# Performance work log

Measured on AMD Instinct MI355X. Metric: run time of the kernel, lower is better.

## Reference

```python
import jax, jax.numpy as jnp
import numpy as np

DROPOUT_P = 0.5
NUM_NODES = 50000


def _gcn_layer(x, W, b, src, dst, ew, num_nodes):
    # support = x @ W ; out = A_hat @ support + b, with A_hat given as edge list
    h = x @ W                               # [N, out_dim]
    msg = h[src] * ew[:, None]              # [E, out_dim]
    agg = jax.ops.segment_sum(msg, dst, num_segments=num_nodes)  # [N, out_dim]
    return agg + b


def setup_inputs() -> dict:
    key = jax.random.key(0)
    ks = jax.random.split(key, 8)
    N, E, F_in, H, C = NUM_NODES, 800000, 512, 128, 64
    x = jax.random.normal(ks[0], (N, F_in), dtype=jnp.float32)
    edge_weight = jax.random.uniform(ks[1], (E,), dtype=jnp.float32)
    W1 = jax.random.normal(ks[2], (F_in, H), dtype=jnp.float32) * (1.0 / np.sqrt(F_in))
    b1 = jax.random.normal(ks[3], (H,), dtype=jnp.float32) * 0.01
    W2 = jax.random.normal(ks[4], (H, C), dtype=jnp.float32) * (1.0 / np.sqrt(H))
    b2 = jax.random.normal(ks[5], (C,), dtype=jnp.float32) * 0.01
    drop_mask = jax.random.uniform(ks[6], (N, H), dtype=jnp.float32)
    edge_index = jax.random.randint(ks[7], (2, E), 0, N, dtype=jnp.int32)
    return {"x": x, "edge_weight": edge_weight, "W1": W1, "b1": b1,
            "W2": W2, "b2": b2, "drop_mask": drop_mask, "edge_index": edge_index}


def reference(x, edge_weight, W1, b1, W2, b2, drop_mask, edge_index):
    src, dst = edge_index[0], edge_index[1]
    h = _gcn_layer(x, W1, b1, src, dst, edge_weight, NUM_NODES)
    h = jax.nn.relu(h)
    # deterministic inverted dropout using precomputed uniform mask
    keep = (drop_mask >= DROPOUT_P).astype(h.dtype)
    h = h * keep / (1.0 - DROPOUT_P)
    h = _gcn_layer(h, W2, b2, src, dst, edge_weight, NUM_NODES)
    return jax.nn.log_softmax(h, axis=1)
```

## Files before the change

kernel.cpp:

```cpp
#include <hip/hip_runtime.h>
#include <cstdint>
#include <cstddef>

constexpr int FIN = 512;
constexpr int HD  = 128;
constexpr int CD  = 64;

typedef __attribute__((ext_vector_type(8))) short short8;
typedef __attribute__((ext_vector_type(4))) float f32x4;

__device__ inline unsigned short f2bf(float f) {
  unsigned int u = __float_as_uint(f);
  u += 0x7fffu + ((u >> 16) & 1u);
  return (unsigned short)(u >> 16);
}
__device__ inline float bf_lo(unsigned int v) { return __uint_as_float(v << 16); }
__device__ inline float bf_hi(unsigned int v) { return __uint_as_float(v & 0xffff0000u); }
__device__ inline float bf1(unsigned short v) { return __uint_as_float((unsigned int)v << 16); }


__global__ __launch_bounds__(256) void hist_kernel(const int* __restrict__ dst, int E,
                                                   int* __restrict__ cnt) {
  int i = blockIdx.x * 256 + threadIdx.x;
  if (i < E) atomicAdd(&cnt[dst[i]], 1);
}

__global__ __launch_bounds__(256) void scan_a(const int* __restrict__ cnt,
                                              int* __restrict__ bs, int n) {
  __shared__ int sh[256];
  int t = threadIdx.x;
  int base = blockIdx.x * 2048;
  int s = 0;
#pragma unroll
  for (int j = 0; j < 8; ++j) {
    int idx = base + j * 256 + t;
    if (idx < n) s += cnt[idx];
  }
  sh[t] = s;
  __syncthreads();
  for (int o = 128; o > 0; o >>= 1) {
    if (t < o) sh[t] += sh[t + o];
    __syncthreads();
  }
  if (t == 0) bs[blockIdx.x] = sh[0];
}

__global__ __launch_bounds__(64) void scan_b(const int* __restrict__ bs,
                                             int* __restrict__ bo, int nb) {
  int t = threadIdx.x;
  int v = (t < nb) ? bs[t] : 0;
  int own = v;
#pragma unroll
  for (int o = 1; o < 64; o <<= 1) {
    int u = __shfl_up(v, o, 64);
    if (t >= o) v += u;
  }
  if (t < nb) bo[t] = v - own;
}

__global__ __launch_bounds__(256) void scan_c(const int* __restrict__ cnt,
                                              const int* __restrict__ bo,
                                              int* __restrict__ off,
                                              int* __restrict__ cur, int n) {
  __shared__ int sh[256];
  int t = threadIdx.x;
  int base = blockIdx.x * 2048 + t * 8;
  int v[8];
  int local = 0;
#pragma unroll
  for (int j = 0; j < 8; ++j) {
    v[j] = (base + j < n) ? cnt[base + j] : 0;
    local += v[j];
  }
  sh[t] = local;
  __syncthreads();
  for (int o = 1; o < 256; o <<= 1) {
    int u = (t >= o) ? sh[t - o] : 0;
    __syncthreads();
    sh[t] += u;
    __syncthreads();
  }
  int run = sh[t] - local + bo[blockIdx.x];
#pragma unroll
  for (int j = 0; j < 8; ++j) {
    if (base + j < n) { off[base + j] = run; cur[base + j] = run; }
    run += v[j];
  }
}

__global__ __launch_bounds__(256) void scatter_kernel(const int* __restrict__ src,
                                                      const int* __restrict__ dst,
                                                      const float* __restrict__ ew, int E,
                                                      int* __restrict__ cur,
                                                      int2* __restrict__ sew) {
  int i = blockIdx.x * 256 + threadIdx.x;
  if (i < E) {
    int d = dst[i];
    int p = atomicAdd(&cur[d], 1);
    sew[p] = make_int2(src[i], __float_as_int(ew[i]));
  }
}


__global__ __launch_bounds__(256) void wprep(const float* __restrict__ W1,
                                             const float* __restrict__ W2,
                                             unsigned short* __restrict__ w1t,
                                             unsigned short* __restrict__ w2t) {
  int idx = blockIdx.x * 256 + threadIdx.x;
  if (idx < FIN * HD) {
    int k = idx >> 7, n = idx & 127;
    w1t[(size_t)n * FIN + k] = f2bf(W1[idx]);
  } else {
    int j = idx - FIN * HD;
    if (j < HD * CD) {
      int k = j >> 6, n = j & 63;
      w2t[(size_t)n * HD + k] = f2bf(W2[j]);
    }
  }
}


__global__ __launch_bounds__(256) void gemm1_mfma(const float* __restrict__ x,
                                                  const unsigned short* __restrict__ w1t,
                                                  unsigned short* __restrict__ h1b, int M) {
  __shared__ unsigned short As[128][40];
  __shared__ unsigned short Bs[128][40];
  const int t    = threadIdx.x;
  const int wave = t >> 6;
  const int lane = t & 63;
  const int l15  = lane & 15;
  const int quad = lane >> 4;
  const int m0   = blockIdx.x * 128;

  const int sr = t >> 1;
  const int sk = (t & 1) * 16;

  const bool aok = (m0 + sr) < M;
  const float* xrow = x + (size_t)(m0 + sr) * FIN + sk;
  const unsigned short* brow = w1t + (size_t)sr * FIN + sk;

  f32x4 acc[2][8];
#pragma unroll
  for (int i = 0; i < 2; ++i)
#pragma unroll
    for (int j = 0; j < 8; ++j) acc[i][j] = (f32x4)0.f;

  for (int k0 = 0; k0 < FIN; k0 += 32) {
    float4 a0 = make_float4(0.f, 0.f, 0.f, 0.f), a1 = a0, a2 = a0, a3 = a0;
    if (aok) {
      a0 = *(const float4*)(xrow + k0);
      a1 = *(const float4*)(xrow + k0 + 4);
      a2 = *(const float4*)(xrow + k0 + 8);
      a3 = *(const float4*)(xrow + k0 + 12);
    }
    uint4 b0 = *(const uint4*)(brow + k0);
    uint4 b1 = *(const uint4*)(brow + k0 + 8);
    __syncthreads();
    unsigned short tmp[16];
    tmp[0]  = f2bf(a0.x); tmp[1]  = f2bf(a0.y); tmp[2]  = f2bf(a0.z); tmp[3]  = f2bf(a0.w);
    tmp[4]  = f2bf(a1.x); tmp[5]  = f2bf(a1.y); tmp[6]  = f2bf(a1.z); tmp[7]  = f2bf(a1.w);
    tmp[8]  = f2bf(a2.x); tmp[9]  = f2bf(a2.y); tmp[10] = f2bf(a2.z); tmp[11] = f2bf(a2.w);
    tmp[12] = f2bf(a3.x); tmp[13] = f2bf(a3.y); tmp[14] = f2bf(a3.z); tmp[15] = f2bf(a3.w);
    *(uint4*)&As[sr][sk]     = ((const uint4*)tmp)[0];
    *(uint4*)&As[sr][sk + 8] = ((const uint4*)tmp)[1];
    *(uint4*)&Bs[sr][sk]     = b0;
    *(uint4*)&Bs[sr][sk + 8] = b1;
    __syncthreads();
    short8 af0 = *(const short8*)&As[wave * 32 + l15][quad * 8];
    short8 af1 = *(const short8*)&As[wave * 32 + 16 + l15][quad * 8];
#pragma unroll
    for (int nt = 0; nt < 8; ++nt) {
      short8 bf = *(const short8*)&Bs[nt * 16 + l15][quad * 8];
      acc[0][nt] = __builtin_amdgcn_mfma_f32_16x16x32_bf16(af0, bf, acc[0][nt], 0, 0, 0);
      acc[1][nt] = __builtin_amdgcn_mfma_f32_16x16x32_bf16(af1, bf, acc[1][nt], 0, 0, 0);
    }
  }
#pragma unroll
  for (int mt = 0; mt < 2; ++mt) {
    const int row0 = m0 + wave * 32 + mt * 16 + quad * 4;
#pragma unroll
    for (int r = 0; r < 4; ++r) {
      int row = row0 + r;
      if (row < M) {
        unsigned short* orow = h1b + (size_t)row * HD + l15;
#pragma unroll
        for (int nt = 0; nt < 8; ++nt) orow[nt * 16] = f2bf(acc[mt][nt][r]);
      }
    }
  }
}


__global__ __launch_bounds__(256) void agg1_kernel(const unsigned int* __restrict__ h1b,
                                                   const float* __restrict__ b1,
                                                   const float* __restrict__ dm,
                                                   const int* __restrict__ off,
                                                   const int* __restrict__ cnt,
                                                   const int2* __restrict__ sew,
                                                   unsigned int* __restrict__ hbf, int N) {
  const int wave = threadIdx.x >> 6;
  const int lane = threadIdx.x & 63;
  const int node = blockIdx.x * 4 + wave;
  if (node >= N) return;
  const int start = off[node];
  const int deg   = cnt[node];
  const int2* ep  = sew + start;

  float a0 = 0.f, a1 = 0.f, c0 = 0.f, c1 = 0.f;
  int e = 0;
  for (; e + 4 <= deg; e += 4) {
    int2 p0 = ep[e + 0];
    int2 p1 = ep[e + 1];
    int2 p2 = ep[e + 2];
    int2 p3 = ep[e + 3];
    unsigned int v0 = h1b[(size_t)p0.x * 64 + lane];
    unsigned int v1 = h1b[(size_t)p1.x * 64 + lane];
    unsigned int v2 = h1b[(size_t)p2.x * 64 + lane];
    unsigned int v3 = h1b[(size_t)p3.x * 64 + lane];
    float w0 = __int_as_float(p0.y), w1 = __int_as_float(p1.y);
    float w2 = __int_as_float(p2.y), w3 = __int_as_float(p3.y);
    a0 = fmaf(bf_lo(v0), w0, a0); a1 = fmaf(bf_hi(v0), w0, a1);
    c0 = fmaf(bf_lo(v1), w1, c0); c1 = fmaf(bf_hi(v1), w1, c1);
    a0 = fmaf(bf_lo(v2), w2, a0); a1 = fmaf(bf_hi(v2), w2, a1);
    c0 = fmaf(bf_lo(v3), w3, c0); c1 = fmaf(bf_hi(v3), w3, c1);
  }
  for (; e < deg; ++e) {
    int2 p = ep[e];
    unsigned int v = h1b[(size_t)p.x * 64 + lane];
    float w = __int_as_float(p.y);
    a0 = fmaf(bf_lo(v), w, a0); a1 = fmaf(bf_hi(v), w, a1);
  }
  a0 += c0; a1 += c1;

  const int f0 = lane * 2;
  float2 bb = *(const float2*)(b1 + f0);
  float2 dd = *(const float2*)(dm + (size_t)node * HD + f0);
  float r0 = fmaxf(a0 + bb.x, 0.f) * ((dd.x >= 0.5f) ? 2.0f : 0.0f);
  float r1 = fmaxf(a1 + bb.y, 0.f) * ((dd.y >= 0.5f) ? 2.0f : 0.0f);
  hbf[(size_t)node * 64 + lane] = (unsigned int)f2bf(r0) | ((unsigned int)f2bf(r1) << 16);
}


__global__ __launch_bounds__(256) void gemm2_mfma(const unsigned short* __restrict__ hbf,
                                                  const unsigned short* __restrict__ w2t,
                                                  unsigned short* __restrict__ h2b, int M) {
  __shared__ unsigned short As[128][40];
  __shared__ unsigned short Bs[64][40];
  const int t    = threadIdx.x;
  const int wave = t >> 6;
  const int lane = t & 63;
  const int l15  = lane & 15;
  const int quad = lane >> 4;
  const int m0   = blockIdx.x * 128;

  const int sr = t >> 1;
  const int sk = (t & 1) * 16;
  const int rb = t >> 2;
  const int kb = (t & 3) * 8;

  const bool aok = (m0 + sr) < M;
  const unsigned short* arow = hbf + (size_t)(m0 + sr) * HD + sk;
  const unsigned short* brow = w2t + (size_t)rb * HD + kb;

  f32x4 acc[2][4];
#pragma unroll
  for (int i = 0; i < 2; ++i)
#pragma unroll
    for (int j = 0; j < 4; ++j) acc[i][j] = (f32x4)0.f;

  for (int k0 = 0; k0 < HD; k0 += 32) {
    uint4 av0 = make_uint4(0, 0, 0, 0), av1 = av0;
    if (aok) {
      av0 = *(const uint4*)(arow + k0);
      av1 = *(const uint4*)(arow + k0 + 8);
    }
    uint4 bv = *(const uint4*)(brow + k0);
    __syncthreads();
    *(uint4*)&As[sr][sk]     = av0;
    *(uint4*)&As[sr][sk + 8] = av1;
    *(uint4*)&Bs[rb][kb]     = bv;
    __syncthreads();
    short8 af0 = *(const short8*)&As[wave * 32 + l15][quad * 8];
    short8 af1 = *(const short8*)&As[wave * 32 + 16 + l15][quad * 8];
#pragma unroll
    for (int nt = 0; nt < 4; ++nt) {
      short8 bf = *(const short8*)&Bs[nt * 16 + l15][quad * 8];
      acc[0][nt] = __builtin_amdgcn_mfma_f32_16x16x32_bf16(af0, bf, acc[0][nt], 0, 0, 0);
      acc[1][nt] = __builtin_amdgcn_mfma_f32_16x16x32_bf16(af1, bf, acc[1][nt], 0, 0, 0);
    }
  }
#pragma unroll
  for (int mt = 0; mt < 2; ++mt) {
    const int row0 = m0 + wave * 32 + mt * 16 + quad * 4;
#pragma unroll
    for (int r = 0; r < 4; ++r) {
      int row = row0 + r;
      if (row < M) {
        unsigned short* orow = h2b + (size_t)row * CD + l15;
#pragma unroll
        for (int nt = 0; nt < 4; ++nt) orow[nt * 16] = f2bf(acc[mt][nt][r]);
      }
    }
  }
}


__global__ __launch_bounds__(256) void agg2_kernel(const unsigned short* __restrict__ h2b,
                                                   const float* __restrict__ b2,
                                                   const int* __restrict__ off,
                                                   const int* __restrict__ cnt,
                                                   const int2* __restrict__ sew,
                                                   float* __restrict__ out, int N) {
  const int wave = threadIdx.x >> 6;
  const int c    = threadIdx.x & 63;
  const int node = blockIdx.x * 4 + wave;
  if (node >= N) return;
  const int start = off[node];
  const int deg   = cnt[node];
  const int2* ep  = sew + start;

  float acc = b2[c], acc2 = 0.f;
  int e = 0;
  for (; e + 4 <= deg; e += 4) {
    int2 p0 = ep[e + 0];
    int2 p1 = ep[e + 1];
    int2 p2 = ep[e + 2];
    int2 p3 = ep[e + 3];
    float v0 = bf1(h2b[(size_t)p0.x * CD + c]);
    float v1 = bf1(h2b[(size_t)p1.x * CD + c]);
    float v2 = bf1(h2b[(size_t)p2.x * CD + c]);
    float v3 = bf1(h2b[(size_t)p3.x * CD + c]);
    acc  = fmaf(v0, __int_as_float(p0.y), acc);
    acc2 = fmaf(v1, __int_as_float(p1.y), acc2);
    acc  = fmaf(v2, __int_as_float(p2.y), acc);
    acc2 = fmaf(v3, __int_as_float(p3.y), acc2);
  }
  for (; e < deg; ++e) {
    int2 p = ep[e];
    acc = fmaf(bf1(h2b[(size_t)p.x * CD + c]), __int_as_float(p.y), acc);
  }
  acc += acc2;

  float m = acc;
#pragma unroll
  for (int o = 32; o > 0; o >>= 1) m = fmaxf(m, __shfl_xor(m, o, 64));
  float ex = __expf(acc - m);
  float ssum = ex;
#pragma unroll
  for (int o = 32; o > 0; o >>= 1) ssum += __shfl_xor(ssum, o, 64);
  out[(size_t)node * CD + c] = (acc - m) - __logf(ssum);
}


extern "C" void kernel_launch(void* const* d_in, const int* in_sizes, int n_in,
                              void* d_out, int out_size, void* d_ws, size_t ws_size,
                              hipStream_t stream) {
  const float* x  = (const float*)d_in[0];
  const float* ew = (const float*)d_in[1];
  const float* W1 = (const float*)d_in[2];
  const float* b1 = (const float*)d_in[3];
  const float* W2 = (const float*)d_in[4];
  const float* b2 = (const float*)d_in[5];
  const float* dm = (const float*)d_in[6];
  const int*   ei = (const int*)d_in[7];
  float* out = (float*)d_out;

  const int E = in_sizes[1];
  const int N = in_sizes[6] / HD;
  const int* srcp = ei;
  const int* dstp = ei + E;
  const int nb = (N + 2047) / 2048;

  uint8_t* w = (uint8_t*)d_ws;
  size_t o = 0;
  auto alloc = [&](size_t bytes) -> void* {
    void* p = w + o;
    o = (o + bytes + 255) & ~(size_t)255;
    return p;
  };
  int*   off  = (int*)alloc((size_t)N * 4);
  int*   cnt  = (int*)alloc((size_t)N * 4);
  int*   cur  = (int*)alloc((size_t)N * 4);
  int2*  sew  = (int2*)alloc((size_t)E * 8);
  unsigned short* h1b = (unsigned short*)alloc((size_t)N * HD * 2);
  unsigned int*   hbf = (unsigned int*)alloc((size_t)N * HD * 2);
  unsigned short* h2b = (unsigned short*)alloc((size_t)N * CD * 2);
  unsigned short* w1t = (unsigned short*)alloc((size_t)FIN * HD * 2);
  unsigned short* w2t = (unsigned short*)alloc((size_t)HD * CD * 2);
  int*   bsum = (int*)alloc((size_t)nb * 4);
  int*   boff = (int*)alloc((size_t)nb * 4);

  hipMemsetAsync(cnt, 0, (size_t)N * 4, stream);
  wprep<<<(FIN * HD + HD * CD + 255) / 256, 256, 0, stream>>>(W1, W2, w1t, w2t);
  hist_kernel<<<(E + 255) / 256, 256, 0, stream>>>(dstp, E, cnt);
  scan_a<<<nb, 256, 0, stream>>>(cnt, bsum, N);
  scan_b<<<1, 64, 0, stream>>>(bsum, boff, nb);
  scan_c<<<nb, 256, 0, stream>>>(cnt, boff, off, cur, N);
  scatter_kernel<<<(E + 255) / 256, 256, 0, stream>>>(srcp, dstp, ew, E, cur, sew);
  gemm1_mfma<<<(N + 127) / 128, 256, 0, stream>>>(x, w1t, h1b, N);
  agg1_kernel<<<(N + 3) / 4, 256, 0, stream>>>((const unsigned int*)h1b, b1, dm, off, cnt, sew, hbf, N);
  gemm2_mfma<<<(N + 127) / 128, 256, 0, stream>>>((const unsigned short*)hbf, w2t, h2b, N);
  agg2_kernel<<<(N + 3) / 4, 256, 0, stream>>>(h2b, b2, off, cnt, sew, out, N);
}
```

Measured before the change: 372.2 us.

## Fuse agg1 with gemm2, chain-scan offsets, and fold memset into prep

Measured after the change: 410.3 us. 10.3% more time.

```diff
diff --git a/kernel.cpp b/kernel.cpp
--- a/kernel.cpp
+++ b/kernel.cpp
@@ -19,52 +19,48 @@
 __device__ inline float bf1(unsigned short v) { return __uint_as_float((unsigned int)v << 16); }
 
 
+__global__ __launch_bounds__(256) void prep(const float* __restrict__ W1,
+                                            const float* __restrict__ W2,
+                                            unsigned short* __restrict__ w1t,
+                                            unsigned short* __restrict__ w2t,
+                                            int* __restrict__ cnt,
+                                            int* __restrict__ ticket,
+                                            int* __restrict__ flag, int n, int nb) {
+  int idx = blockIdx.x * 256 + threadIdx.x;
+  if (idx < FIN * HD) {
+    int k = idx >> 7, c = idx & 127;
+    w1t[(size_t)c * FIN + k] = f2bf(W1[idx]);
+  } else if (idx < FIN * HD + HD * CD) {
+    int j = idx - FIN * HD;
+    int k = j >> 6, c = j & 63;
+    w2t[(size_t)c * HD + k] = f2bf(W2[j]);
+  }
+  if (idx < n) cnt[idx] = 0;
+  else if (idx < n + nb) flag[idx - n] = 0;
+  else if (idx == n + nb) *ticket = 0;
+}
+
+
 __global__ __launch_bounds__(256) void hist_kernel(const int* __restrict__ dst, int E,
                                                    int* __restrict__ cnt) {
   int i = blockIdx.x * 256 + threadIdx.x;
   if (i < E) atomicAdd(&cnt[dst[i]], 1);
 }
 
-__global__ __launch_bounds__(256) void scan_a(const int* __restrict__ cnt,
-                                              int* __restrict__ bs, int n) {
+
+__global__ __launch_bounds__(256) void scan_chain(const int* __restrict__ cnt,
+                                                  int* __restrict__ off,
+                                                  int* __restrict__ cur, int n,
+                                                  int* __restrict__ ticket,
+                                                  int* __restrict__ partial,
+                                                  int* __restrict__ flag) {
   __shared__ int sh[256];
+  __shared__ int sbid, sprev;
   int t = threadIdx.x;
-  int base = blockIdx.x * 2048;
-  int s = 0;
-#pragma unroll
-  for (int j = 0; j < 8; ++j) {
-    int idx = base + j * 256 + t;
-    if (idx < n) s += cnt[idx];
-  }
-  sh[t] = s;
+  if (t == 0) sbid = atomicAdd(ticket, 1);
   __syncthreads();
-  for (int o = 128; o > 0; o >>= 1) {
-    if (t < o) sh[t] += sh[t + o];
-    __syncthreads();
-  }
-  if (t == 0) bs[blockIdx.x] = sh[0];
-}
-
-__global__ __launch_bounds__(64) void scan_b(const int* __restrict__ bs,
-                                             int* __restrict__ bo, int nb) {
-  int t = threadIdx.x;
-  int v = (t < nb) ? bs[t] : 0;
-  int own = v;
-#pragma unroll
-  for (int o = 1; o < 64; o <<= 1) {
-    int u = __shfl_up(v, o, 64);
-    if (t >= o) v += u;
-  }
-  if (t < nb) bo[t] = v - own;
-}
-
-__global__ __launch_bounds__(256) void scan_c(const int* __restrict__ cnt,
-                                              const int* __restrict__ bo,
-                                              int* __restrict__ off,
-                                              int* __restrict__ cur, int n) {
-  __shared__ int sh[256];
-  int t = threadIdx.x;
-  int base = blockIdx.x * 2048 + t * 8;
+  const int bid  = sbid;
+  const int base = bid * 2048 + t * 8;
   int v[8];
   int local = 0;
 #pragma unroll
@@ -80,13 +76,26 @@
     sh[t] += u;
     __syncthreads();
   }
-  int run = sh[t] - local + bo[blockIdx.x];
+  if (t == 0) {
+    int prev = 0;
+    if (bid > 0) {
+      while (__hip_atomic_load(&flag[bid - 1], __ATOMIC_ACQUIRE,
+                               __HIP_MEMORY_SCOPE_AGENT) != 1) {}
+      prev = partial[bid - 1];
+    }
+    partial[bid] = prev + sh[255];
+    __hip_atomic_store(&flag[bid], 1, __ATOMIC_RELEASE, __HIP_MEMORY_SCOPE_AGENT);
+    sprev = prev;
+  }
+  __syncthreads();
+  int run = sprev + sh[t] - local;
 #pragma unroll
   for (int j = 0; j < 8; ++j) {
     if (base + j < n) { off[base + j] = run; cur[base + j] = run; }
     run += v[j];
   }
 }
+
 
 __global__ __launch_bounds__(256) void scatter_kernel(const int* __restrict__ src,
                                                       const int* __restrict__ dst,
@@ -98,24 +107,6 @@
     int d = dst[i];
     int p = atomicAdd(&cur[d], 1);
     sew[p] = make_int2(src[i], __float_as_int(ew[i]));
-  }
-}
-
-
-__global__ __launch_bounds__(256) void wprep(const float* __restrict__ W1,
-                                             const float* __restrict__ W2,
-                                             unsigned short* __restrict__ w1t,
-                                             unsigned short* __restrict__ w2t) {
-  int idx = blockIdx.x * 256 + threadIdx.x;
-  if (idx < FIN * HD) {
-    int k = idx >> 7, n = idx & 127;
-    w1t[(size_t)n * FIN + k] = f2bf(W1[idx]);
-  } else {
-    int j = idx - FIN * HD;
-    if (j < HD * CD) {
-      int k = j >> 6, n = j & 63;
-      w2t[(size_t)n * HD + k] = f2bf(W2[j]);
-    }
   }
 }
 
@@ -191,115 +182,118 @@
 }
 
 
-__global__ __launch_bounds__(256) void agg1_kernel(const unsigned int* __restrict__ h1b,
-                                                   const float* __restrict__ b1,
-                                                   const float* __restrict__ dm,
-                                                   const int* __restrict__ off,
-                                                   const int* __restrict__ cnt,
-                                                   const int2* __restrict__ sew,
-                                                   unsigned int* __restrict__ hbf, int N) {
-  const int wave = threadIdx.x >> 6;
-  const int lane = threadIdx.x & 63;
-  const int node = blockIdx.x * 4 + wave;
-  if (node >= N) return;
-  const int start = off[node];
-  const int deg   = cnt[node];
-  const int2* ep  = sew + start;
-
-  float a0 = 0.f, a1 = 0.f, c0 = 0.f, c1 = 0.f;
-  int e = 0;
-  for (; e + 4 <= deg; e += 4) {
-    int2 p0 = ep[e + 0];
-    int2 p1 = ep[e + 1];
-    int2 p2 = ep[e + 2];
-    int2 p3 = ep[e + 3];
-    unsigned int v0 = h1b[(size_t)p0.x * 64 + lane];
-    unsigned int v1 = h1b[(size_t)p1.x * 64 + lane];
-    unsigned int v2 = h1b[(size_t)p2.x * 64 + lane];
-    unsigned int v3 = h1b[(size_t)p3.x * 64 + lane];
-    float w0 = __int_as_float(p0.y), w1 = __int_as_float(p1.y);
-    float w2 = __int_as_float(p2.y), w3 = __int_as_float(p3.y);
-    a0 = fmaf(bf_lo(v0), w0, a0); a1 = fmaf(bf_hi(v0), w0, a1);
-    c0 = fmaf(bf_lo(v1), w1, c0); c1 = fmaf(bf_hi(v1), w1, c1);
-    a0 = fmaf(bf_lo(v2), w2, a0); a1 = fmaf(bf_hi(v2), w2, a1);
-    c0 = fmaf(bf_lo(v3), w3, c0); c1 = fmaf(bf_hi(v3), w3, c1);
-  }
-  for (; e < deg; ++e) {
-    int2 p = ep[e];
-    unsigned int v = h1b[(size_t)p.x * 64 + lane];
-    float w = __int_as_float(p.y);
-    a0 = fmaf(bf_lo(v), w, a0); a1 = fmaf(bf_hi(v), w, a1);
-  }
-  a0 += c0; a1 += c1;
-
-  const int f0 = lane * 2;
-  float2 bb = *(const float2*)(b1 + f0);
-  float2 dd = *(const float2*)(dm + (size_t)node * HD + f0);
-  float r0 = fmaxf(a0 + bb.x, 0.f) * ((dd.x >= 0.5f) ? 2.0f : 0.0f);
-  float r1 = fmaxf(a1 + bb.y, 0.f) * ((dd.y >= 0.5f) ? 2.0f : 0.0f);
-  hbf[(size_t)node * 64 + lane] = (unsigned int)f2bf(r0) | ((unsigned int)f2bf(r1) << 16);
-}
-
-
-__global__ __launch_bounds__(256) void gemm2_mfma(const unsigned short* __restrict__ hbf,
+__global__ __launch_bounds__(256) void agg1_gemm2(const unsigned int* __restrict__ h1b,
+                                                  const float* __restrict__ b1,
+                                                  const float* __restrict__ dm,
+                                                  const int* __restrict__ off,
+                                                  const int* __restrict__ cnt,
+                                                  const int2* __restrict__ sew,
                                                   const unsigned short* __restrict__ w2t,
-                                                  unsigned short* __restrict__ h2b, int M) {
-  __shared__ unsigned short As[128][40];
-  __shared__ unsigned short Bs[64][40];
+                                                  unsigned short* __restrict__ h2b, int N) {
+  __shared__ unsigned short As[64][136];
+  __shared__ unsigned short Bs[64][136];
   const int t    = threadIdx.x;
   const int wave = t >> 6;
   const int lane = t & 63;
   const int l15  = lane & 15;
   const int quad = lane >> 4;
-  const int m0   = blockIdx.x * 128;
-
-  const int sr = t >> 1;
-  const int sk = (t & 1) * 16;
-  const int rb = t >> 2;
-  const int kb = (t & 3) * 8;
-
-  const bool aok = (m0 + sr) < M;
-  const unsigned short* arow = hbf + (size_t)(m0 + sr) * HD + sk;
-  const unsigned short* brow = w2t + (size_t)rb * HD + kb;
-
-  f32x4 acc[2][4];
-#pragma unroll
-  for (int i = 0; i < 2; ++i)
-#pragma unroll
-    for (int j = 0; j < 4; ++j) acc[i][j] = (f32x4)0.f;
-
-  for (int k0 = 0; k0 < HD; k0 += 32) {
-    uint4 av0 = make_uint4(0, 0, 0, 0), av1 = av0;
-    if (aok) {
-      av0 = *(const uint4*)(arow + k0);
-      av1 = *(const uint4*)(arow + k0 + 8);
-    }
-    uint4 bv = *(const uint4*)(brow + k0);
-    __syncthreads();
-    *(uint4*)&As[sr][sk]     = av0;
-    *(uint4*)&As[sr][sk + 8] = av1;
-    *(uint4*)&Bs[rb][kb]     = bv;
-    __syncthreads();
-    short8 af0 = *(const short8*)&As[wave * 32 + l15][quad * 8];
-    short8 af1 = *(const short8*)&As[wave * 32 + 16 + l15][quad * 8];
+  const int m0   = blockIdx.x * 64;
+
+  {
+    const int rb = t >> 2, kb = (t & 3) * 32;
+    const unsigned short* srcp = w2t + (size_t)rb * HD + kb;
+#pragma unroll
+    for (int j = 0; j < 4; ++j)
+      *(uint4*)&Bs[rb][kb + j * 8] = *(const uint4*)(srcp + j * 8);
+  }
+
+  for (int i = 0; i < 16; ++i) {
+    const int row  = wave * 16 + i;
+    const int node = m0 + row;
+    unsigned int pack = 0;
+    if (node < N) {
+      const int start = off[node];
+      const int deg   = cnt[node];
+      const int2* ep  = sew + start;
+      float a0 = 0.f, a1 = 0.f, c0 = 0.f, c1 = 0.f;
+      float e0 = 0.f, e1 = 0.f, g0 = 0.f, g1 = 0.f;
+      int e = 0;
+      for (; e + 8 <= deg; e += 8) {
+        int2 p0 = ep[e + 0], p1 = ep[e + 1], p2 = ep[e + 2], p3 = ep[e + 3];
+        int2 p4 = ep[e + 4], p5 = ep[e + 5], p6 = ep[e + 6], p7 = ep[e + 7];
+        unsigned int v0 = h1b[(size_t)p0.x * 64 + lane];
+        unsigned int v1 = h1b[(size_t)p1.x * 64 + lane];
+        unsigned int v2 = h1b[(size_t)p2.x * 64 + lane];
+        unsigned int v3 = h1b[(size_t)p3.x * 64 + lane];
+        unsigned int v4 = h1b[(size_t)p4.x * 64 + lane];
+        unsigned int v5 = h1b[(size_t)p5.x * 64 + lane];
+        unsigned int v6 = h1b[(size_t)p6.x * 64 + lane];
+        unsigned int v7 = h1b[(size_t)p7.x * 64 + lane];
+        float w0 = __int_as_float(p0.y), w1 = __int_as_float(p1.y);
+        float w2 = __int_as_float(p2.y), w3 = __int_as_float(p3.y);
+        float w4 = __int_as_float(p4.y), w5 = __int_as_float(p5.y);
+        float w6 = __int_as_float(p6.y), w7 = __int_as_float(p7.y);
+        a0 = fmaf(bf_lo(v0), w0, a0); a1 = fmaf(bf_hi(v0), w0, a1);
+        c0 = fmaf(bf_lo(v1), w1, c0); c1 = fmaf(bf_hi(v1), w1, c1);
+        e0 = fmaf(bf_lo(v2), w2, e0); e1 = fmaf(bf_hi(v2), w2, e1);
+        g0 = fmaf(bf_lo(v3), w3, g0); g1 = fmaf(bf_hi(v3), w3, g1);
+        a0 = fmaf(bf_lo(v4), w4, a0); a1 = fmaf(bf_hi(v4), w4, a1);
+        c0 = fmaf(bf_lo(v5), w5, c0); c1 = fmaf(bf_hi(v5), w5, c1);
+        e0 = fmaf(bf_lo(v6), w6, e0); e1 = fmaf(bf_hi(v6), w6, e1);
+        g0 = fmaf(bf_lo(v7), w7, g0); g1 = fmaf(bf_hi(v7), w7, g1);
+      }
+      for (; e + 4 <= deg; e += 4) {
+        int2 p0 = ep[e + 0], p1 = ep[e + 1], p2 = ep[e + 2], p3 = ep[e + 3];
+        unsigned int v0 = h1b[(size_t)p0.x * 64 + lane];
+        unsigned int v1 = h1b[(size_t)p1.x * 64 + lane];
+        unsigned int v2 = h1b[(size_t)p2.x * 64 + lane];
+        unsigned int v3 = h1b[(size_t)p3.x * 64 + lane];
+        float w0 = __int_as_float(p0.y), w1 = __int_as_float(p1.y);
+        float w2 = __int_as_float(p2.y), w3 = __int_as_float(p3.y);
+        a0 = fmaf(bf_lo(v0), w0, a0); a1 = fmaf(bf_hi(v0), w0, a1);
+        c0 = fmaf(bf_lo(v1), w1, c0); c1 = fmaf(bf_hi(v1), w1, c1);
+        e0 = fmaf(bf_lo(v2), w2, e0); e1 = fmaf(bf_hi(v2), w2, e1);
+        g0 = fmaf(bf_lo(v3), w3, g0); g1 = fmaf(bf_hi(v3), w3, g1);
+      }
+      for (; e < deg; ++e) {
+        int2 p = ep[e];
+        unsigned int v = h1b[(size_t)p.x * 64 + lane];
+        float w = __int_as_float(p.y);
+        a0 = fmaf(bf_lo(v), w, a0); a1 = fmaf(bf_hi(v), w, a1);
+      }
+      a0 += c0 + e0 + g0; a1 += c1 + e1 + g1;
+      const int f0 = lane * 2;
+      float2 bb = *(const float2*)(b1 + f0);
+      float2 dd = *(const float2*)(dm + (size_t)node * HD + f0);
+      float r0 = fmaxf(a0 + bb.x, 0.f) * ((dd.x >= 0.5f) ? 2.0f : 0.0f);
+      float r1 = fmaxf(a1 + bb.y, 0.f) * ((dd.y >= 0.5f) ? 2.0f : 0.0f);
+      pack = (unsigned int)f2bf(r0) | ((unsigned int)f2bf(r1) << 16);
+    }
+    *(unsigned int*)&As[row][lane * 2] = pack;
+  }
+  __syncthreads();
+
+  f32x4 acc[4];
+#pragma unroll
+  for (int nt = 0; nt < 4; ++nt) acc[nt] = (f32x4)0.f;
+#pragma unroll
+  for (int ks = 0; ks < 4; ++ks) {
+    const int k0 = ks * 32 + quad * 8;
+    short8 af = *(const short8*)&As[wave * 16 + l15][k0];
 #pragma unroll
     for (int nt = 0; nt < 4; ++nt) {
-      short8 bf = *(const short8*)&Bs[nt * 16 + l15][quad * 8];
-      acc[0][nt] = __builtin_amdgcn_mfma_f32_16x16x32_bf16(af0, bf, acc[0][nt], 0, 0, 0);
-      acc[1][nt] = __builtin_amdgcn_mfma_f32_16x16x32_bf16(af1, bf, acc[1][nt], 0, 0, 0);
-    }
-  }
-#pragma unroll
-  for (int mt = 0; mt < 2; ++mt) {
-    const int row0 = m0 + wave * 32 + mt * 16 + quad * 4;
-#pragma unroll
-    for (int r = 0; r < 4; ++r) {
-      int row = row0 + r;
-      if (row < M) {
-        unsigned short* orow = h2b + (size_t)row * CD + l15;
-#pragma unroll
-        for (int nt = 0; nt < 4; ++nt) orow[nt * 16] = f2bf(acc[mt][nt][r]);
-      }
+      short8 bf = *(const short8*)&Bs[nt * 16 + l15][k0];
+      acc[nt] = __builtin_amdgcn_mfma_f32_16x16x32_bf16(af, bf, acc[nt], 0, 0, 0);
+    }
+  }
+  const int row0 = m0 + wave * 16 + quad * 4;
+#pragma unroll
+  for (int r = 0; r < 4; ++r) {
+    int row = row0 + r;
+    if (row < N) {
+      unsigned short* orow = h2b + (size_t)row * CD + l15;
+#pragma unroll
+      for (int nt = 0; nt < 4; ++nt) orow[nt * 16] = f2bf(acc[nt][r]);
     }
   }
 }
@@ -319,27 +313,44 @@
   const int deg   = cnt[node];
   const int2* ep  = sew + start;
 
-  float acc = b2[c], acc2 = 0.f;
+  float acc = b2[c], a1 = 0.f, a2 = 0.f, a3 = 0.f;
   int e = 0;
-  for (; e + 4 <= deg; e += 4) {
-    int2 p0 = ep[e + 0];
-    int2 p1 = ep[e + 1];
-    int2 p2 = ep[e + 2];
-    int2 p3 = ep[e + 3];
+  for (; e + 8 <= deg; e += 8) {
+    int2 p0 = ep[e + 0], p1 = ep[e + 1], p2 = ep[e + 2], p3 = ep[e + 3];
+    int2 p4 = ep[e + 4], p5 = ep[e + 5], p6 = ep[e + 6], p7 = ep[e + 7];
     float v0 = bf1(h2b[(size_t)p0.x * CD + c]);
     float v1 = bf1(h2b[(size_t)p1.x * CD + c]);
     float v2 = bf1(h2b[(size_t)p2.x * CD + c]);
     float v3 = bf1(h2b[(size_t)p3.x * CD + c]);
-    acc  = fmaf(v0, __int_as_float(p0.y), acc);
-    acc2 = fmaf(v1, __int_as_float(p1.y), acc2);
-    acc  = fmaf(v2, __int_as_float(p2.y), acc);
-    acc2 = fmaf(v3, __int_as_float(p3.y), acc2);
+    float v4 = bf1(h2b[(size_t)p4.x * CD + c]);
+    float v5 = bf1(h2b[(size_t)p5.x * CD + c]);
+    float v6 = bf1(h2b[(size_t)p6.x * CD + c]);
+    float v7 = bf1(h2b[(size_t)p7.x * CD + c]);
+    acc = fmaf(v0, __int_as_float(p0.y), acc);
+    a1  = fmaf(v1, __int_as_float(p1.y), a1);
+    a2  = fmaf(v2, __int_as_float(p2.y), a2);
+    a3  = fmaf(v3, __int_as_float(p3.y), a3);
+    acc = fmaf(v4, __int_as_float(p4.y), acc);
+    a1  = fmaf(v5, __int_as_float(p5.y), a1);
+    a2  = fmaf(v6, __int_as_float(p6.y), a2);
+    a3  = fmaf(v7, __int_as_float(p7.y), a3);
+  }
+  for (; e + 4 <= deg; e += 4) {
+    int2 p0 = ep[e + 0], p1 = ep[e + 1], p2 = ep[e + 2], p3 = ep[e + 3];
+    float v0 = bf1(h2b[(size_t)p0.x * CD + c]);
+    float v1 = bf1(h2b[(size_t)p1.x * CD + c]);
+    float v2 = bf1(h2b[(size_t)p2.x * CD + c]);
+    float v3 = bf1(h2b[(size_t)p3.x * CD + c]);
+    acc = fmaf(v0, __int_as_float(p0.y), acc);
+    a1  = fmaf(v1, __int_as_float(p1.y), a1);
+    a2  = fmaf(v2, __int_as_float(p2.y), a2);
+    a3  = fmaf(v3, __int_as_float(p3.y), a3);
   }
   for (; e < deg; ++e) {
     int2 p = ep[e];
     acc = fmaf(bf1(h2b[(size_t)p.x * CD + c]), __int_as_float(p.y), acc);
   }
-  acc += acc2;
+  acc += a1 + a2 + a3;
 
   float m = acc;
 #pragma unroll
@@ -378,27 +389,24 @@
     o = (o + bytes + 255) & ~(size_t)255;
     return p;
   };
-  int*   off  = (int*)alloc((size_t)N * 4);
-  int*   cnt  = (int*)alloc((size_t)N * 4);
-  int*   cur  = (int*)alloc((size_t)N * 4);
-  int2*  sew  = (int2*)alloc((size_t)E * 8);
+  int*   off    = (int*)alloc((size_t)N * 4);
+  int*   cnt    = (int*)alloc((size_t)N * 4);
+  int*   cur    = (int*)alloc((size_t)N * 4);
+  int2*  sew    = (int2*)alloc((size_t)E * 8);
   unsigned short* h1b = (unsigned short*)alloc((size_t)N * HD * 2);
-  unsigned int*   hbf = (unsigned int*)alloc((size_t)N * HD * 2);
   unsigned short* h2b = (unsigned short*)alloc((size_t)N * CD * 2);
   unsigned short* w1t = (unsigned short*)alloc((size_t)FIN * HD * 2);
   unsigned short* w2t = (unsigned short*)alloc((size_t)HD * CD * 2);
-  int*   bsum = (int*)alloc((size_t)nb * 4);
-  int*   boff = (int*)alloc((size_t)nb * 4);
-
-  hipMemsetAsync(cnt, 0, (size_t)N * 4, stream);
-  wprep<<<(FIN * HD + HD * CD + 255) / 256, 256, 0, stream>>>(W1, W2, w1t, w2t);
+  int*   ticket  = (int*)alloc(4);
+  int*   partial = (int*)alloc((size_t)nb * 4);
+  int*   flag    = (int*)alloc((size_t)nb * 4);
+
+  const int prep_threads = FIN * HD + HD * CD;
+  prep<<<(prep_threads + 255) / 256, 256, 0, stream>>>(W1, W2, w1t, w2t, cnt, ticket, flag, N, nb);
   hist_kernel<<<(E + 255) / 256, 256, 0, stream>>>(dstp, E, cnt);
-  scan_a<<<nb, 256, 0, stream>>>(cnt, bsum, N);
-  scan_b<<<1, 64, 0, stream>>>(bsum, boff, nb);
-  scan_c<<<nb, 256, 0, stream>>>(cnt, boff, off, cur, N);
+  scan_chain<<<nb, 256, 0, stream>>>(cnt, off, cur, N, ticket, partial, flag);
   scatter_kernel<<<(E + 255) / 256, 256, 0, stream>>>(srcp, dstp, ew, E, cur, sew);
   gemm1_mfma<<<(N + 127) / 128, 256, 0, stream>>>(x, w1t, h1b, N);
-  agg1_kernel<<<(N + 3) / 4, 256, 0, stream>>>((const unsigned int*)h1b, b1, dm, off, cnt, sew, hbf, N);
-  gemm2_mfma<<<(N + 127) / 128, 256, 0, stream>>>((const unsigned short*)hbf, w2t, h2b, N);
+  agg1_gemm2<<<(N + 63) / 64, 256, 0, stream>>>((const unsigned int*)h1b, b1, dm, off, cnt, sew, w2t, h2b, N);
   agg2_kernel<<<(N + 3) / 4, 256, 0, stream>>>(h2b, b2, off, cnt, sew, out, N);
 }
```
